# Optimization experiments

Hardware: AMD Instinct MI355X
Metric: run time of the kernel (lower is better)

## Reference

```python
import jax, jax.numpy as jnp
import numpy as np

EPS = 1e-6
N_LEVELS = 8
BASE_RES = 16
DESIRED_RES = 128
N_POINTS = 524288


def _grid_meta():
    # replicate DAGrid.__init__ level resolutions and flat-table offsets
    b = (DESIRED_RES / BASE_RES) ** (1.0 / (N_LEVELS - 1))
    scales, offsets = [], [0]
    for i in range(N_LEVELS):
        res = int(BASE_RES * b ** i)
        scales.append(res)
        offsets.append(offsets[-1] + (res + 1) ** 3)
    return scales, offsets


def setup_inputs() -> dict:
    key = jax.random.key(0)
    scales, offsets = _grid_meta()
    lo = np.array([-1.0, -1.0, -1.0], np.float32)
    hi_eps = np.array([1.0, 1.0, 1.0], np.float32) - EPS  # bounds[1] -= eps before anchor init
    anchors = []
    for res in scales:
        axes = [np.linspace(lo[d], hi_eps[d], res + 1, dtype=np.float32) for d in range(3)]
        g = np.stack(np.meshgrid(*axes, indexing='ij'), axis=-1).reshape(-1, 3)
        anchors.append(g)
    data = jnp.asarray(np.concatenate(anchors, axis=0))  # (T, 3) learned grid param
    xyz = jax.random.normal(key, (N_POINTS, 3), dtype=jnp.float32)
    return {
        'xyz': xyz,
        'data': data,
        'scales': jnp.asarray(scales, jnp.float32),              # (L,)
        'level_offsets': jnp.asarray(offsets[:-1], jnp.int32),   # (L,)
        'bounds': jnp.asarray(np.stack([lo, np.array([1.0, 1.0, 1.0], np.float32)])),  # (2,3) raw bbox
    }


def reference(xyz, data, scales, level_offsets, bounds):
    L = scales.shape[0]
    lo = bounds[0]
    hi = bounds[1] - EPS
    size = jnp.max(bounds[1] - bounds[0])
    x = jnp.clip(xyz, lo, hi)
    xn = (x - lo) / size                                   # (N,3) in [0,1)
    fx = xn[None, :, :] * scales[:, None, None]            # (L,N,3)
    base = jnp.floor(fx).astype(jnp.int32)                 # (L,N,3) lower corner
    off = fx - base.astype(fx.dtype)                       # (L,N,3) trilinear frac
    corners = jnp.asarray([[0, 0, 0], [0, 0, 1], [0, 1, 0], [0, 1, 1],
                           [1, 0, 0], [1, 0, 1], [1, 1, 0], [1, 1, 1]], jnp.int32)  # (8,3)
    idx = base[:, :, None, :] + corners[None, None, :, :]  # (L,N,8,3)
    r1 = (scales + 1.0).astype(jnp.int32)                  # (L,) points per axis
    ind = (idx[..., 0] * (r1 * r1)[:, None, None]
           + idx[..., 1] * r1[:, None, None]
           + idx[..., 2]
           + level_offsets[:, None, None])                 # (L,N,8) flat gather index
    val = data[ind]                                        # (L,N,8,3) gathered anchors
    cf = corners.astype(fx.dtype)
    w = jnp.clip(1.0 - cf + (2.0 * cf - 1.0) * off[:, :, None, :], 0.0, 1.0)  # (L,N,8,3)
    w = w[..., 0] * w[..., 1] * w[..., 2]                  # (L,N,8) trilinear weights
    freqs = (2.0 ** jnp.arange(L, dtype=fx.dtype))[:, None, None, None]
    enc = jnp.concatenate([jnp.sin(val * freqs), jnp.cos(val * freqs)], axis=-1)  # (L,N,8,6)
    out = jnp.einsum('lnk,lnkf->nlf', w, enc)              # (N,L,6)
    out = out.reshape(xyz.shape[0], -1)                    # (N, 6*L)
    return jnp.concatenate([xyz, out], axis=-1)            # (N, 3 + 6*L)
```

## Files before the change

### kernel.cpp

```cpp
#include <hip/hip_runtime.h>

#define NLEV 8
#define PTS_PER_BLOCK 32
#define ROW_F 51

__global__ __launch_bounds__(256) void phase_repack(
    const float* __restrict__ data,
    const int*   __restrict__ level_offsets,
    uint4* __restrict__ tab, int T)
{
    __shared__ float sv[(256 + 1) * 3];
    __shared__ int   soff[NLEV];
    const int tid  = threadIdx.x;
    const int base = blockIdx.x * 256;

    if (tid < NLEV) soff[tid] = level_offsets[tid];
    for (int k = tid; k < (256 + 1) * 3; k += 256) {
        const int gi = base * 3 + k;
        sv[k] = (gi < T * 3) ? data[gi] : 0.0f;
    }
    __syncthreads();

    const int i = base + tid;
    if (i >= T) return;

    int l = 0;
    #pragma unroll
    for (int j = 1; j < NLEV; ++j) l += (i >= soff[j]) ? 1 : 0;
    const float s = exp2f((float)l) * 0.15915494309189535f;

    unsigned q[6];
    #pragma unroll
    for (int k = 0; k < 6; ++k) {
        float f = sv[tid * 3 + k] * s;
        f -= floorf(f);
        const unsigned v = (unsigned)(f * 65536.0f + 0.5f);
        q[k] = v & 0xffffu;
    }
    tab[i] = make_uint4(q[0] | (q[1] << 16), q[2], q[3] | (q[4] << 16), q[5]);
}

__device__ __forceinline__ void sincos_rev(float r, float& sn, float& cs) {
    asm volatile("v_sin_f32 %0, %1" : "=v"(sn) : "v"(r));
    asm volatile("v_cos_f32 %0, %1" : "=v"(cs) : "v"(r));
}

__global__ __launch_bounds__(256) void dagrid_kernel(
    const float* __restrict__ xyz,
    const uint4* __restrict__ tab,
    const float* __restrict__ scales,
    const int*   __restrict__ level_offsets,
    const float* __restrict__ bounds,
    float* __restrict__ out,
    int npts)
{
    __shared__ alignas(16) float sxyz[PTS_PER_BLOCK * 3];
    __shared__ alignas(16) float sres[PTS_PER_BLOCK][ROW_F];

    const int tid = threadIdx.x;
    const int l   = tid & 7;
    const int p   = tid >> 3;
    const int block_base = blockIdx.x * PTS_PER_BLOCK;
    const bool full_block = (block_base + PTS_PER_BLOCK <= npts);

    if (full_block) {
        if (tid < 24)
            ((float4*)sxyz)[tid] = ((const float4*)(xyz + (size_t)block_base * 3))[tid];
    } else if (tid < PTS_PER_BLOCK * 3) {
        const int gi = block_base * 3 + tid;
        sxyz[tid] = (gi < npts * 3) ? xyz[gi] : 0.0f;
    }

    const float scale = scales[l];
    const int   off_l = level_offsets[l];

    const float lox = bounds[0], loy = bounds[1], loz = bounds[2];
    const float hix = bounds[3] - 1e-6f;
    const float hiy = bounds[4] - 1e-6f;
    const float hiz = bounds[5] - 1e-6f;
    const float size = fmaxf(fmaxf(bounds[3] - bounds[0], bounds[4] - bounds[1]),
                             bounds[5] - bounds[2]);
    const float inv_size = 1.0f / size;

    __syncthreads();

    const int n = block_base + p;
    const bool active = (n < npts);

    const float rx = sxyz[p * 3 + 0];
    const float ry = sxyz[p * 3 + 1];
    const float rz = sxyz[p * 3 + 2];

    float acc0 = 0.f, acc1 = 0.f, acc2 = 0.f, acc3 = 0.f, acc4 = 0.f, acc5 = 0.f;

    if (active) {
        const float x = fminf(fmaxf(rx, lox), hix);
        const float y = fminf(fmaxf(ry, loy), hiy);
        const float z = fminf(fmaxf(rz, loz), hiz);
        const float xn = (x - lox) * inv_size;
        const float yn = (y - loy) * inv_size;
        const float zn = (z - loz) * inv_size;

        const int r1   = (int)scale + 1;
        const int r1sq = r1 * r1;

        const float fx = xn * scale;
        const float fy = yn * scale;
        const float fz = zn * scale;
        const float bxf = floorf(fx), byf = floorf(fy), bzf = floorf(fz);
        const float ox = fx - bxf;
        const float oy = fy - byf;
        const float oz = fz - bzf;

        const int i000 = (int)bxf * r1sq + (int)byf * r1 + (int)bzf + off_l;

        const uint4 e0 = tab[i000];
        const uint4 e1 = tab[i000 + r1];
        const uint4 e2 = tab[i000 + r1sq];
        const uint4 e3 = tab[i000 + r1sq + r1];

        const float wz0 = 1.0f - oz;
        const float wx1 = ox, wx0 = 1.0f - ox;
        const float wy1 = oy, wy0 = 1.0f - oy;
        const float K = 1.0f / 65536.0f;

        float sn, cs;
        #define PAIRE(e, WXY)                                                        \
        {                                                                            \
            const float w0 = (WXY) * wz0;                                            \
            const float w1 = (WXY) * oz;                                             \
            sincos_rev((float)(e.x & 0xffffu) * K, sn, cs); acc0 += w0*sn; acc3 += w0*cs; \
            sincos_rev((float)(e.x >> 16)     * K, sn, cs); acc1 += w0*sn; acc4 += w0*cs; \
            sincos_rev((float)(e.y & 0xffffu) * K, sn, cs); acc2 += w0*sn; acc5 += w0*cs; \
            sincos_rev((float)(e.z & 0xffffu) * K, sn, cs); acc0 += w1*sn; acc3 += w1*cs; \
            sincos_rev((float)(e.z >> 16)     * K, sn, cs); acc1 += w1*sn; acc4 += w1*cs; \
            sincos_rev((float)(e.w & 0xffffu) * K, sn, cs); acc2 += w1*sn; acc5 += w1*cs; \
        }
        PAIRE(e0, wx0 * wy0)
        PAIRE(e1, wx0 * wy1)
        PAIRE(e2, wx1 * wy0)
        PAIRE(e3, wx1 * wy1)
        #undef PAIRE
    }

    {
        float* row = sres[p];
        const int c = 3 + l * 6;
        row[c + 0] = acc0; row[c + 1] = acc1; row[c + 2] = acc2;
        row[c + 3] = acc3; row[c + 4] = acc4; row[c + 5] = acc5;
        if (l == 0) { row[0] = rx; row[1] = ry; row[2] = rz; }
    }
    __syncthreads();

    if (full_block) {
        const float4* flat4 = (const float4*)&sres[0][0];
        float4* ob4 = (float4*)(out + (size_t)block_base * ROW_F);
        for (int i = tid; i < (PTS_PER_BLOCK * ROW_F) / 4; i += 256)
            ob4[i] = flat4[i];
    } else {
        const float* flat = &sres[0][0];
        float* ob = out + (size_t)block_base * ROW_F;
        const int lim = npts * ROW_F - block_base * ROW_F;
        for (int i = tid; i < PTS_PER_BLOCK * ROW_F; i += 256)
            if (i < lim) ob[i] = flat[i];
    }
}

typedef float f4u __attribute__((ext_vector_type(4), aligned(4)));
typedef float f2u __attribute__((ext_vector_type(2), aligned(4)));

__global__ __launch_bounds__(256) void dagrid_kernel_direct(
    const float* __restrict__ xyz,
    const float* __restrict__ data,
    const float* __restrict__ scales,
    const int*   __restrict__ level_offsets,
    const float* __restrict__ bounds,
    float* __restrict__ out,
    int npts)
{
    __shared__ alignas(16) float sxyz[PTS_PER_BLOCK * 3];
    __shared__ alignas(16) float sres[PTS_PER_BLOCK][ROW_F];

    const int tid = threadIdx.x;
    const int l   = tid & 7;
    const int p   = tid >> 3;
    const int block_base = blockIdx.x * PTS_PER_BLOCK;

    if (tid < PTS_PER_BLOCK * 3) {
        const int gi = block_base * 3 + tid;
        sxyz[tid] = (gi < npts * 3) ? xyz[gi] : 0.0f;
    }
    const float scale = scales[l];
    const int   off_l = level_offsets[l];
    const float lox = bounds[0], loy = bounds[1], loz = bounds[2];
    const float hix = bounds[3] - 1e-6f;
    const float hiy = bounds[4] - 1e-6f;
    const float hiz = bounds[5] - 1e-6f;
    const float size = fmaxf(fmaxf(bounds[3] - bounds[0], bounds[4] - bounds[1]),
                             bounds[5] - bounds[2]);
    const float inv_size = 1.0f / size;
    __syncthreads();

    const int n = block_base + p;
    const bool active = (n < npts);
    const float rx = sxyz[p * 3 + 0];
    const float ry = sxyz[p * 3 + 1];
    const float rz = sxyz[p * 3 + 2];
    float acc0 = 0.f, acc1 = 0.f, acc2 = 0.f, acc3 = 0.f, acc4 = 0.f, acc5 = 0.f;

    if (active) {
        const float x = fminf(fmaxf(rx, lox), hix);
        const float y = fminf(fmaxf(ry, loy), hiy);
        const float z = fminf(fmaxf(rz, loz), hiz);
        const float xn = (x - lox) * inv_size;
        const float yn = (y - loy) * inv_size;
        const float zn = (z - loz) * inv_size;
        const int r1 = (int)scale + 1;
        const int r1sq = r1 * r1;
        const float fx = xn * scale, fy = yn * scale, fz = zn * scale;
        const float bxf = floorf(fx), byf = floorf(fy), bzf = floorf(fz);
        const float ox = fx - bxf, oy = fy - byf, oz = fz - bzf;
        const int i000 = (int)bxf * r1sq + (int)byf * r1 + (int)bzf + off_l;
        const float* p0 = data + 3 * (size_t)i000;
        const float* p1 = p0 + 3 * r1;
        const float* p2 = p0 + 3 * r1sq;
        const float* p3 = p2 + 3 * r1;
        const f4u a0 = *(const f4u*)p0;  const f2u b0 = *(const f2u*)(p0 + 4);
        const f4u a1 = *(const f4u*)p1;  const f2u b1 = *(const f2u*)(p1 + 4);
        const f4u a2 = *(const f4u*)p2;  const f2u b2 = *(const f2u*)(p2 + 4);
        const f4u a3 = *(const f4u*)p3;  const f2u b3 = *(const f2u*)(p3 + 4);
        const float freq = (float)(1 << l);
        const float wz0 = 1.0f - oz;
        const float wx1 = ox, wx0 = 1.0f - ox;
        const float wy1 = oy, wy0 = 1.0f - oy;
        float sn, cs;
        #define PAIR(a, b, WXY)                                                   \
        {                                                                         \
            const float w0 = (WXY) * wz0;                                         \
            const float w1 = (WXY) * oz;                                          \
            __sincosf(a.x * freq, &sn, &cs); acc0 += w0 * sn; acc3 += w0 * cs;    \
            __sincosf(a.y * freq, &sn, &cs); acc1 += w0 * sn; acc4 += w0 * cs;    \
            __sincosf(a.z * freq, &sn, &cs); acc2 += w0 * sn; acc5 += w0 * cs;    \
            __sincosf(a.w * freq, &sn, &cs); acc0 += w1 * sn; acc3 += w1 * cs;    \
            __sincosf(b.x * freq, &sn, &cs); acc1 += w1 * sn; acc4 += w1 * cs;    \
            __sincosf(b.y * freq, &sn, &cs); acc2 += w1 * sn; acc5 += w1 * cs;    \
        }
        PAIR(a0, b0, wx0 * wy0)
        PAIR(a1, b1, wx0 * wy1)
        PAIR(a2, b2, wx1 * wy0)
        PAIR(a3, b3, wx1 * wy1)
        #undef PAIR
    }
    {
        float* row = sres[p];
        const int c = 3 + l * 6;
        row[c + 0] = acc0; row[c + 1] = acc1; row[c + 2] = acc2;
        row[c + 3] = acc3; row[c + 4] = acc4; row[c + 5] = acc5;
        if (l == 0) { row[0] = rx; row[1] = ry; row[2] = rz; }
    }
    __syncthreads();
    {
        const float* flat = &sres[0][0];
        float* ob = out + (size_t)block_base * ROW_F;
        const int lim = npts * ROW_F - block_base * ROW_F;
        for (int i = tid; i < PTS_PER_BLOCK * ROW_F; i += 256)
            if (i < lim) ob[i] = flat[i];
    }
}

extern "C" void kernel_launch(void* const* d_in, const int* in_sizes, int n_in,
                              void* d_out, int out_size, void* d_ws, size_t ws_size,
                              hipStream_t stream) {
    const float* xyz           = (const float*)d_in[0];
    const float* data          = (const float*)d_in[1];
    const float* scales        = (const float*)d_in[2];
    const int*   level_offsets = (const int*)d_in[3];
    const float* bounds        = (const float*)d_in[4];
    float* out = (float*)d_out;

    const int npts = in_sizes[0] / 3;
    const int T    = in_sizes[1] / 3;
    const int nblocks = (npts + PTS_PER_BLOCK - 1) / PTS_PER_BLOCK;

    const size_t ws_needed = (size_t)T * sizeof(uint4);
    if (d_ws != nullptr && ws_size >= ws_needed) {
        uint4* tab = (uint4*)d_ws;
        phase_repack<<<(T + 255) / 256, 256, 0, stream>>>(data, level_offsets, tab, T);
        dagrid_kernel<<<nblocks, 256, 0, stream>>>(xyz, tab, scales, level_offsets,
                                                   bounds, out, npts);
    } else {
        dagrid_kernel_direct<<<nblocks, 256, 0, stream>>>(xyz, data, scales,
                                                          level_offsets, bounds,
                                                          out, npts);
    }
}
```

Baseline: 153.1 us.

## Shrink phase table to 8 bytes per anchor and process two points per thread

The repack kernel now stores only one anchor's three 16-bit phases per 8-byte entry instead of a 16-byte entry holding an anchor plus its z-neighbor. The main kernel reads adjacent z-pairs with an 8-byte-aligned 16-byte load, which halves the table footprint and the repack write traffic. Each thread now handles two points (64 points per block), giving more independent gathers in flight per thread and fewer blocks. The asm volatile qualifiers are dropped so the compiler can schedule the sin/cos instructions. Costs are higher register pressure, and inactive points now clamp to index 0 and gather anyway.

Result: faster. 129.2 us (-15.6%).

```diff
diff --git a/kernel.cpp b/kernel.cpp
--- a/kernel.cpp
+++ b/kernel.cpp
@@ -1,21 +1,23 @@
 #include <hip/hip_runtime.h>
 
 #define NLEV 8
-#define PTS_PER_BLOCK 32
+#define PTS_PER_BLOCK 64
 #define ROW_F 51
 
-__global__ __launch_bounds__(256) void phase_repack(
+typedef unsigned int u4a8 __attribute__((ext_vector_type(4), aligned(8)));
+
+__global__ __launch_bounds__(256) void phase_repack8(
     const float* __restrict__ data,
     const int*   __restrict__ level_offsets,
-    uint4* __restrict__ tab, int T)
+    uint2* __restrict__ tab, int T)
 {
-    __shared__ float sv[(256 + 1) * 3];
+    __shared__ float sv[256 * 3];
     __shared__ int   soff[NLEV];
     const int tid  = threadIdx.x;
     const int base = blockIdx.x * 256;
 
     if (tid < NLEV) soff[tid] = level_offsets[tid];
-    for (int k = tid; k < (256 + 1) * 3; k += 256) {
+    for (int k = tid; k < 256 * 3; k += 256) {
         const int gi = base * 3 + k;
         sv[k] = (gi < T * 3) ? data[gi] : 0.0f;
     }
@@ -27,27 +29,26 @@
     int l = 0;
     #pragma unroll
     for (int j = 1; j < NLEV; ++j) l += (i >= soff[j]) ? 1 : 0;
-    const float s = exp2f((float)l) * 0.15915494309189535f;
-
-    unsigned q[6];
+    const float s = (float)(1 << l) * 0.15915494309189535f;
+
+    unsigned q[3];
     #pragma unroll
-    for (int k = 0; k < 6; ++k) {
+    for (int k = 0; k < 3; ++k) {
         float f = sv[tid * 3 + k] * s;
         f -= floorf(f);
-        const unsigned v = (unsigned)(f * 65536.0f + 0.5f);
-        q[k] = v & 0xffffu;
-    }
-    tab[i] = make_uint4(q[0] | (q[1] << 16), q[2], q[3] | (q[4] << 16), q[5]);
+        q[k] = ((unsigned)(f * 65536.0f + 0.5f)) & 0xffffu;
+    }
+    tab[i] = make_uint2(q[0] | (q[1] << 16), q[2]);
 }
 
 __device__ __forceinline__ void sincos_rev(float r, float& sn, float& cs) {
-    asm volatile("v_sin_f32 %0, %1" : "=v"(sn) : "v"(r));
-    asm volatile("v_cos_f32 %0, %1" : "=v"(cs) : "v"(r));
+    asm("v_sin_f32 %0, %1" : "=v"(sn) : "v"(r));
+    asm("v_cos_f32 %0, %1" : "=v"(cs) : "v"(r));
 }
 
 __global__ __launch_bounds__(256) void dagrid_kernel(
     const float* __restrict__ xyz,
-    const uint4* __restrict__ tab,
+    const uint2* __restrict__ tab,
     const float* __restrict__ scales,
     const int*   __restrict__ level_offsets,
     const float* __restrict__ bounds,
@@ -64,7 +65,7 @@
     const bool full_block = (block_base + PTS_PER_BLOCK <= npts);
 
     if (full_block) {
-        if (tid < 24)
+        if (tid < 48)
             ((float4*)sxyz)[tid] = ((const float4*)(xyz + (size_t)block_base * 3))[tid];
     } else if (tid < PTS_PER_BLOCK * 3) {
         const int gi = block_base * 3 + tid;
@@ -84,71 +85,92 @@
 
     __syncthreads();
 
-    const int n = block_base + p;
-    const bool active = (n < npts);
-
-    const float rx = sxyz[p * 3 + 0];
-    const float ry = sxyz[p * 3 + 1];
-    const float rz = sxyz[p * 3 + 2];
-
-    float acc0 = 0.f, acc1 = 0.f, acc2 = 0.f, acc3 = 0.f, acc4 = 0.f, acc5 = 0.f;
-
-    if (active) {
-        const float x = fminf(fmaxf(rx, lox), hix);
-        const float y = fminf(fmaxf(ry, loy), hiy);
-        const float z = fminf(fmaxf(rz, loz), hiz);
-        const float xn = (x - lox) * inv_size;
-        const float yn = (y - loy) * inv_size;
-        const float zn = (z - loz) * inv_size;
-
-        const int r1   = (int)scale + 1;
-        const int r1sq = r1 * r1;
-
-        const float fx = xn * scale;
-        const float fy = yn * scale;
-        const float fz = zn * scale;
-        const float bxf = floorf(fx), byf = floorf(fy), bzf = floorf(fz);
-        const float ox = fx - bxf;
-        const float oy = fy - byf;
-        const float oz = fz - bzf;
-
-        const int i000 = (int)bxf * r1sq + (int)byf * r1 + (int)bzf + off_l;
-
-        const uint4 e0 = tab[i000];
-        const uint4 e1 = tab[i000 + r1];
-        const uint4 e2 = tab[i000 + r1sq];
-        const uint4 e3 = tab[i000 + r1sq + r1];
-
-        const float wz0 = 1.0f - oz;
-        const float wx1 = ox, wx0 = 1.0f - ox;
-        const float wy1 = oy, wy0 = 1.0f - oy;
-        const float K = 1.0f / 65536.0f;
-
-        float sn, cs;
-        #define PAIRE(e, WXY)                                                        \
-        {                                                                            \
-            const float w0 = (WXY) * wz0;                                            \
-            const float w1 = (WXY) * oz;                                             \
-            sincos_rev((float)(e.x & 0xffffu) * K, sn, cs); acc0 += w0*sn; acc3 += w0*cs; \
-            sincos_rev((float)(e.x >> 16)     * K, sn, cs); acc1 += w0*sn; acc4 += w0*cs; \
-            sincos_rev((float)(e.y & 0xffffu) * K, sn, cs); acc2 += w0*sn; acc5 += w0*cs; \
-            sincos_rev((float)(e.z & 0xffffu) * K, sn, cs); acc0 += w1*sn; acc3 += w1*cs; \
-            sincos_rev((float)(e.z >> 16)     * K, sn, cs); acc1 += w1*sn; acc4 += w1*cs; \
-            sincos_rev((float)(e.w & 0xffffu) * K, sn, cs); acc2 += w1*sn; acc5 += w1*cs; \
+    const int nA = block_base + p;
+    const int nB = nA + 32;
+    const bool actA = (nA < npts);
+    const bool actB = (nB < npts);
+
+    const float rxA = sxyz[p * 3 + 0], ryA = sxyz[p * 3 + 1], rzA = sxyz[p * 3 + 2];
+    const float rxB = sxyz[(p + 32) * 3 + 0], ryB = sxyz[(p + 32) * 3 + 1],
+                rzB = sxyz[(p + 32) * 3 + 2];
+
+    const int r1   = (int)scale + 1;
+    const int r1sq = r1 * r1;
+
+    #define ADDR(rx, ry, rz, act, ox, oy, oz, idx)                                \
+    {                                                                             \
+        const float x = fminf(fmaxf(rx, lox), hix);                               \
+        const float y = fminf(fmaxf(ry, loy), hiy);                               \
+        const float z = fminf(fmaxf(rz, loz), hiz);                               \
+        const float fx = (x - lox) * inv_size * scale;                            \
+        const float fy = (y - loy) * inv_size * scale;                            \
+        const float fz = (z - loz) * inv_size * scale;                            \
+        const float bxf = floorf(fx), byf = floorf(fy), bzf = floorf(fz);         \
+        ox = fx - bxf; oy = fy - byf; oz = fz - bzf;                              \
+        idx = act ? ((int)bxf * r1sq + (int)byf * r1 + (int)bzf + off_l) : 0;     \
+    }
+    float oxA, oyA, ozA, oxB, oyB, ozB;
+    int idxA, idxB;
+    ADDR(rxA, ryA, rzA, actA, oxA, oyA, ozA, idxA)
+    ADDR(rxB, ryB, rzB, actB, oxB, oyB, ozB, idxB)
+    #undef ADDR
+
+    const u4a8 eA0 = *(const u4a8*)(tab + idxA);
+    const u4a8 eA1 = *(const u4a8*)(tab + idxA + r1);
+    const u4a8 eA2 = *(const u4a8*)(tab + idxA + r1sq);
+    const u4a8 eA3 = *(const u4a8*)(tab + idxA + r1sq + r1);
+    const u4a8 eB0 = *(const u4a8*)(tab + idxB);
+    const u4a8 eB1 = *(const u4a8*)(tab + idxB + r1);
+    const u4a8 eB2 = *(const u4a8*)(tab + idxB + r1sq);
+    const u4a8 eB3 = *(const u4a8*)(tab + idxB + r1sq + r1);
+
+    const float K = 1.0f / 65536.0f;
+
+    #define PAIRE(e, WXY, oz_, wz0_, a0, a1, a2, a3, a4, a5)                      \
+    {                                                                             \
+        const float w0 = (WXY) * (wz0_);                                          \
+        const float w1 = (WXY) * (oz_);                                           \
+        float sn, cs;                                                             \
+        sincos_rev((float)(e.x & 0xffffu) * K, sn, cs); a0 += w0*sn; a3 += w0*cs; \
+        sincos_rev((float)(e.x >> 16)     * K, sn, cs); a1 += w0*sn; a4 += w0*cs; \
+        sincos_rev((float)(e.y)           * K, sn, cs); a2 += w0*sn; a5 += w0*cs; \
+        sincos_rev((float)(e.z & 0xffffu) * K, sn, cs); a0 += w1*sn; a3 += w1*cs; \
+        sincos_rev((float)(e.z >> 16)     * K, sn, cs); a1 += w1*sn; a4 += w1*cs; \
+        sincos_rev((float)(e.w)           * K, sn, cs); a2 += w1*sn; a5 += w1*cs; \
+    }
+
+    float a0 = 0.f, a1 = 0.f, a2 = 0.f, a3 = 0.f, a4 = 0.f, a5 = 0.f;
+    {
+        const float wz0 = 1.0f - ozA;
+        const float wx0 = 1.0f - oxA, wy0 = 1.0f - oyA;
+        PAIRE(eA0, wx0 * wy0, ozA, wz0, a0, a1, a2, a3, a4, a5)
+        PAIRE(eA1, wx0 * oyA, ozA, wz0, a0, a1, a2, a3, a4, a5)
+        PAIRE(eA2, oxA * wy0, ozA, wz0, a0, a1, a2, a3, a4, a5)
+        PAIRE(eA3, oxA * oyA, ozA, wz0, a0, a1, a2, a3, a4, a5)
+    }
+    float b0 = 0.f, b1 = 0.f, b2 = 0.f, b3 = 0.f, b4 = 0.f, b5 = 0.f;
+    {
+        const float wz0 = 1.0f - ozB;
+        const float wx0 = 1.0f - oxB, wy0 = 1.0f - oyB;
+        PAIRE(eB0, wx0 * wy0, ozB, wz0, b0, b1, b2, b3, b4, b5)
+        PAIRE(eB1, wx0 * oyB, ozB, wz0, b0, b1, b2, b3, b4, b5)
+        PAIRE(eB2, oxB * wy0, ozB, wz0, b0, b1, b2, b3, b4, b5)
+        PAIRE(eB3, oxB * oyB, ozB, wz0, b0, b1, b2, b3, b4, b5)
+    }
+    #undef PAIRE
+
+    {
+        const int c = 3 + l * 6;
+        float* rowA = sres[p];
+        rowA[c + 0] = a0; rowA[c + 1] = a1; rowA[c + 2] = a2;
+        rowA[c + 3] = a3; rowA[c + 4] = a4; rowA[c + 5] = a5;
+        float* rowB = sres[p + 32];
+        rowB[c + 0] = b0; rowB[c + 1] = b1; rowB[c + 2] = b2;
+        rowB[c + 3] = b3; rowB[c + 4] = b4; rowB[c + 5] = b5;
+        if (l == 0) {
+            rowA[0] = rxA; rowA[1] = ryA; rowA[2] = rzA;
+            rowB[0] = rxB; rowB[1] = ryB; rowB[2] = rzB;
         }
-        PAIRE(e0, wx0 * wy0)
-        PAIRE(e1, wx0 * wy1)
-        PAIRE(e2, wx1 * wy0)
-        PAIRE(e3, wx1 * wy1)
-        #undef PAIRE
-    }
-
-    {
-        float* row = sres[p];
-        const int c = 3 + l * 6;
-        row[c + 0] = acc0; row[c + 1] = acc1; row[c + 2] = acc2;
-        row[c + 3] = acc3; row[c + 4] = acc4; row[c + 5] = acc5;
-        if (l == 0) { row[0] = rx; row[1] = ry; row[2] = rz; }
     }
     __syncthreads();
 
@@ -178,15 +200,15 @@
     float* __restrict__ out,
     int npts)
 {
-    __shared__ alignas(16) float sxyz[PTS_PER_BLOCK * 3];
-    __shared__ alignas(16) float sres[PTS_PER_BLOCK][ROW_F];
+    __shared__ alignas(16) float sxyz[32 * 3];
+    __shared__ alignas(16) float sres[32][ROW_F];
 
     const int tid = threadIdx.x;
     const int l   = tid & 7;
     const int p   = tid >> 3;
-    const int block_base = blockIdx.x * PTS_PER_BLOCK;
-
-    if (tid < PTS_PER_BLOCK * 3) {
+    const int block_base = blockIdx.x * 32;
+
+    if (tid < 32 * 3) {
         const int gi = block_base * 3 + tid;
         sxyz[tid] = (gi < npts * 3) ? xyz[gi] : 0.0f;
     }
@@ -225,10 +247,10 @@
         const float* p1 = p0 + 3 * r1;
         const float* p2 = p0 + 3 * r1sq;
         const float* p3 = p2 + 3 * r1;
-        const f4u a0 = *(const f4u*)p0;  const f2u b0 = *(const f2u*)(p0 + 4);
-        const f4u a1 = *(const f4u*)p1;  const f2u b1 = *(const f2u*)(p1 + 4);
-        const f4u a2 = *(const f4u*)p2;  const f2u b2 = *(const f2u*)(p2 + 4);
-        const f4u a3 = *(const f4u*)p3;  const f2u b3 = *(const f2u*)(p3 + 4);
+        const f4u q0 = *(const f4u*)p0;  const f2u g0 = *(const f2u*)(p0 + 4);
+        const f4u q1 = *(const f4u*)p1;  const f2u g1 = *(const f2u*)(p1 + 4);
+        const f4u q2 = *(const f4u*)p2;  const f2u g2 = *(const f2u*)(p2 + 4);
+        const f4u q3 = *(const f4u*)p3;  const f2u g3 = *(const f2u*)(p3 + 4);
         const float freq = (float)(1 << l);
         const float wz0 = 1.0f - oz;
         const float wx1 = ox, wx0 = 1.0f - ox;
@@ -245,10 +267,10 @@
             __sincosf(b.x * freq, &sn, &cs); acc1 += w1 * sn; acc4 += w1 * cs;    \
             __sincosf(b.y * freq, &sn, &cs); acc2 += w1 * sn; acc5 += w1 * cs;    \
         }
-        PAIR(a0, b0, wx0 * wy0)
-        PAIR(a1, b1, wx0 * wy1)
-        PAIR(a2, b2, wx1 * wy0)
-        PAIR(a3, b3, wx1 * wy1)
+        PAIR(q0, g0, wx0 * wy0)
+        PAIR(q1, g1, wx0 * wy1)
+        PAIR(q2, g2, wx1 * wy0)
+        PAIR(q3, g3, wx1 * wy1)
         #undef PAIR
     }
     {
@@ -263,7 +285,7 @@
         const float* flat = &sres[0][0];
         float* ob = out + (size_t)block_base * ROW_F;
         const int lim = npts * ROW_F - block_base * ROW_F;
-        for (int i = tid; i < PTS_PER_BLOCK * ROW_F; i += 256)
+        for (int i = tid; i < 32 * ROW_F; i += 256)
             if (i < lim) ob[i] = flat[i];
     }
 }
@@ -280,15 +302,16 @@
 
     const int npts = in_sizes[0] / 3;
     const int T    = in_sizes[1] / 3;
-    const int nblocks = (npts + PTS_PER_BLOCK - 1) / PTS_PER_BLOCK;
-
-    const size_t ws_needed = (size_t)T * sizeof(uint4);
+
+    const size_t ws_needed = (size_t)T * sizeof(uint2);
     if (d_ws != nullptr && ws_size >= ws_needed) {
-        uint4* tab = (uint4*)d_ws;
-        phase_repack<<<(T + 255) / 256, 256, 0, stream>>>(data, level_offsets, tab, T);
+        uint2* tab = (uint2*)d_ws;
+        phase_repack8<<<(T + 255) / 256, 256, 0, stream>>>(data, level_offsets, tab, T);
+        const int nblocks = (npts + PTS_PER_BLOCK - 1) / PTS_PER_BLOCK;
         dagrid_kernel<<<nblocks, 256, 0, stream>>>(xyz, tab, scales, level_offsets,
                                                    bounds, out, npts);
     } else {
+        const int nblocks = (npts + 31) / 32;
         dagrid_kernel_direct<<<nblocks, 256, 0, stream>>>(xyz, data, scales,
                                                           level_offsets, bounds,
                                                           out, npts);
```
